# Performance work log

Hardware: AMD Instinct MI355X
Metric: run time of the kernel (lower is better)

## Reference

```python
import jax, jax.numpy as jnp
import numpy as np

DIM = 128
HEADS = 8
DH = DIM // HEADS
WIN = (4, 4, 4)
TOPK = 4
EPS = 1e-6


def _ln(x, g, b):
    mu = jnp.mean(x, -1, keepdims=True)
    var = jnp.mean((x - mu) ** 2, -1, keepdims=True)
    return (x - mu) * jax.lax.rsqrt(var + EPS) * g + b


def _win3d(x, p1, p2, p3):
    # x: [B,S,H,W,C] -> [B, p1*p2*p3, Ms, Mh, Mw, C]
    B, S, H, W, C = x.shape
    Ms, Mh, Mw = S // p1, H // p2, W // p3
    x = x.reshape(B, p1, Ms, p2, Mh, p3, Mw, C)
    x = x.transpose(0, 1, 3, 5, 2, 4, 6, 7)
    return x.reshape(B, p1 * p2 * p3, Ms, Mh, Mw, C)


def setup_inputs() -> dict:
    key = jax.random.key(0)
    ks = jax.random.split(key, 20)

    def lin(k, din, dout):
        return jax.random.normal(k, (din, dout), jnp.float32) * 0.02

    return {
        "x_in": jax.random.normal(ks[0], (2, 128, 16, 32, 32), jnp.float32),
        "x_g_in": jax.random.normal(ks[1], (2, 128, 8, 16, 16), jnp.float32),
        # Atten (global branch)
        "qkv_w": lin(ks[2], DIM, 3 * DIM), "qkv_b": jnp.zeros((3 * DIM,), jnp.float32),
        "proj_w": lin(ks[3], DIM, DIM), "proj_b": jnp.zeros((DIM,), jnp.float32),
        # shared LayerNorm (self.norm1 is reused everywhere in the original)
        "ln_g": jnp.ones((DIM,), jnp.float32), "ln_b": jnp.zeros((DIM,), jnp.float32),
        # mlp (global branch FFN)
        "mlp_w1": lin(ks[4], DIM, 4 * DIM), "mlp_b1": jnp.zeros((4 * DIM,), jnp.float32),
        "mlp_w2": lin(ks[5], 4 * DIM, DIM), "mlp_b2": jnp.zeros((DIM,), jnp.float32),
        # TopkRouting
        "rq_w": lin(ks[6], DIM, DIM), "rq_b": jnp.zeros((DIM,), jnp.float32),
        "rk_w": lin(ks[7], DIM, DIM), "rk_b": jnp.zeros((DIM,), jnp.float32),
        # fused qkv over concatenated local+gathered-global tokens
        "gqkv_w": lin(ks[8], DIM, 3 * DIM), "gqkv_b": jnp.zeros((3 * DIM,), jnp.float32),
        "wo_w": lin(ks[9], DIM, DIM), "wo_b": jnp.zeros((DIM,), jnp.float32),
        # mlp2 (local branch FFN)
        "mlp2_w1": lin(ks[10], DIM, 4 * DIM), "mlp2_b1": jnp.zeros((4 * DIM,), jnp.float32),
        "mlp2_w2": lin(ks[11], 4 * DIM, DIM), "mlp2_b2": jnp.zeros((DIM,), jnp.float32),
    }


def reference(x_in, x_g_in, qkv_w, qkv_b, proj_w, proj_b, ln_g, ln_b,
              mlp_w1, mlp_b1, mlp_w2, mlp_b2, rq_w, rq_b, rk_w, rk_b,
              gqkv_w, gqkv_b, wo_w, wo_b, mlp2_w1, mlp2_b1, mlp2_w2, mlp2_b2):
    B, C, S, H, W = x_in.shape
    Ms, Mh, Mw = WIN
    p1, p2, p3 = S // Ms, H // Mh, W // Mw  # pads are zero for these shapes
    nw, w3l = p1 * p2 * p3, Ms * Mh * Mw
    scale = DIM ** -0.5  # BiLevelRoutingAttention.scale = dim**-0.5 (not per-head)

    x = jnp.transpose(x_in, (0, 2, 3, 4, 1))  # [B,S,H,W,C]
    shortcut_l = _win3d(x, p1, p2, p3).reshape(B, nw, w3l, C)

    # ---- global branch: full self-attention + FFN ----
    _, _, gS, gH, gW = x_g_in.shape
    gN = gS * gH * gW
    xg = jnp.transpose(x_g_in, (0, 2, 3, 4, 1)).reshape(B, gN, C)
    h = _ln(xg, ln_g, ln_b)
    qkv = (h @ qkv_w + qkv_b).reshape(B, gN, 3, HEADS, DH).transpose(2, 0, 3, 1, 4)
    q, k, v = qkv[0], qkv[1], qkv[2]
    a = jax.nn.softmax(jnp.einsum('bhnd,bhmd->bhnm', q, k) * DH ** -0.5, axis=-1)
    o = jnp.einsum('bhnm,bhmd->bhnd', a, v).transpose(0, 2, 1, 3).reshape(B, gN, C)
    xg = (o @ proj_w + proj_b) + xg
    xg4 = xg.reshape(B, gS, gH, gW, C)
    h = _ln(xg4, ln_g, ln_b)
    xg4 = xg4 + (jax.nn.gelu(h @ mlp_w1 + mlp_b1, approximate=False) @ mlp_w2 + mlp_b2)

    # ---- top-k window routing ----
    swg = _win3d(xg4, p1, p2, p3)  # [B,nw,gMs,gMh,gMw,C]
    w3g = swg.shape[2] * swg.shape[3] * swg.shape[4]
    g_win = swg.mean((2, 3, 4))  # [B,nw,C]
    qh = g_win @ rq_w + rq_b
    kh = g_win @ rk_w + rk_b
    logit = jnp.einsum('bnc,bmc->bnm', qh * scale, kh)
    _tvals, tidx = jax.lax.top_k(logit, TOPK)  # r_weight is computed but unused in the original forward

    # gather top-k global windows' tokens per local window
    gflat = swg.reshape(B, nw, w3g, C)
    gath = jax.vmap(lambda kv, idx: kv[idx])(gflat, tidx)  # [B,nw,topk,w3g,C]
    sc = jnp.concatenate([shortcut_l, gath.reshape(B, nw, TOPK * w3g, C)], axis=2)
    w3 = w3l + TOPK * w3g

    # ---- local+routed attention over concatenated tokens ----
    qkvp = _ln(sc, ln_g, ln_b) @ gqkv_w + gqkv_b
    qp, kp, vp = jnp.split(qkvp, 3, axis=-1)
    qp = qp.reshape(B, nw, w3, HEADS, DH)
    kp = kp.reshape(B, nw, w3, HEADS, DH)
    vp = vp.reshape(B, nw, w3, HEADS, DH)
    aw = jax.nn.softmax(jnp.einsum('bnqhd,bnkhd->bnhqk', qp * scale, kp), axis=-1)
    out = jnp.einsum('bnhqk,bnkhd->bnqhd', aw, vp).reshape(B, nw, w3, C)

    l = out[:, :, :w3l] @ wo_w + wo_b + shortcut_l
    l = l.reshape(B, p1, p2, p3, Ms, Mh, Mw, C).transpose(0, 1, 4, 2, 5, 3, 6, 7).reshape(B, S, H, W, C)
    l = l + (jax.nn.gelu(_ln(l, ln_g, ln_b) @ mlp2_w1 + mlp2_b1, approximate=False) @ mlp2_w2 + mlp2_b2)

    l_out = jnp.transpose(l, (0, 4, 1, 2, 3))
    g_out = jnp.transpose(xg4, (0, 4, 1, 2, 3))
    return (l_out, g_out)
```

## Files before the change

kernel.cpp:

```cpp
#include <hip/hip_runtime.h>
#include <hip/hip_bf16.h>
#include <math.h>

#define BATCH 2
#define CDIM 128
#define SS 16
#define HH_ 32
#define WW_ 32
#define NSP (SS*HH_*WW_)
#define GS 8
#define GH 16
#define GW 16
#define GN (GS*GH*GW)
#define HEADS 8
#define DH 16
#define NW 256
#define W3L 64
#define W3G 8
#define TOPK 4
#define W3 (W3L + TOPK*W3G)
#define LN_EPS 1e-6f
#define ROUTE_SCALE 0.08838834764831845f
#define GATTN_SCALE 0.25f

typedef short bshort8 __attribute__((ext_vector_type(8)));
typedef float f32x4 __attribute__((ext_vector_type(4)));

__device__ __forceinline__ unsigned short f2bf(float f) {
    unsigned int u = __float_as_uint(f);
    unsigned int r = (u + 0x7fffu + ((u >> 16) & 1u)) >> 16;
    return (unsigned short)r;
}
__device__ __forceinline__ float gelu_exact(float x) {
    float z = x * 0.70710678118654752f;
    float az = fabsf(z);
    float t = 1.0f / fmaf(0.3275911f, az, 1.0f);
    float poly = t * fmaf(t, fmaf(t, fmaf(t, fmaf(t, 1.061405429f, -1.453152027f),
                     1.421413741f), -0.284496736f), 0.254829592f);
    float e = __expf(-az * az);
    float erfv = 1.0f - poly * e;
    erfv = (z < 0.f) ? -erfv : erfv;
    return 0.5f * x * (1.0f + erfv);
}
__device__ __forceinline__ float shfl_sum32(float v) {
#pragma unroll
    for (int m = 16; m > 0; m >>= 1) v += __shfl_xor(v, m);
    return v;
}
__device__ __forceinline__ float shfl_sum16(float v) {
#pragma unroll
    for (int m = 8; m > 0; m >>= 1) v += __shfl_xor(v, m);
    return v;
}
__device__ __forceinline__ float shfl_sum8(float v) {
#pragma unroll
    for (int m = 4; m > 0; m >>= 1) v += __shfl_xor(v, m);
    return v;
}

__global__ __launch_bounds__(256) void k_prep_fat(const float* __restrict__ gqkv_w,
        const float* __restrict__ m2_w1, const float* __restrict__ m2_w2,
        const float* __restrict__ proj_w, const float* __restrict__ mlp_w1,
        const float* __restrict__ mlp_w2, const float* __restrict__ wo_w,
        const float* __restrict__ qkv_w,
        unsigned short* __restrict__ wt, unsigned short* __restrict__ w1t,
        unsigned short* __restrict__ w2t, unsigned short* __restrict__ projt,
        unsigned short* __restrict__ gw1t, unsigned short* __restrict__ gw2t,
        unsigned short* __restrict__ wot, unsigned short* __restrict__ qkvt,
        const float* __restrict__ x_in, const float* __restrict__ ln_g,
        const float* __restrict__ ln_b, unsigned short* __restrict__ lnsc) {
    __shared__ float tile[16][132];
    int t = threadIdx.x;
    if (blockIdx.x < 192) {
        int id = blockIdx.x * 256 + t;
        int frag = id >> 6, lane = id & 63;
        int l15 = lane & 15, quad = lane >> 4;
        const float* srcw; unsigned short* dstw; int KS, OUT, lf; float sc = 1.f;
        if (frag < 96)        { lf = frag;       srcw = gqkv_w; dstw = wt;    KS = 4;  OUT = 384; if ((lf >> 2) < 8) sc = ROUTE_SCALE; }
        else if (frag < 224)  { lf = frag - 96;  srcw = m2_w1;  dstw = w1t;   KS = 4;  OUT = 512; }
        else if (frag < 352)  { lf = frag - 224; srcw = m2_w2;  dstw = w2t;   KS = 16; OUT = 128; }
        else if (frag < 384)  { lf = frag - 352; srcw = proj_w; dstw = projt; KS = 4;  OUT = 128; }
        else if (frag < 512)  { lf = frag - 384; srcw = mlp_w1; dstw = gw1t;  KS = 4;  OUT = 512; }
        else if (frag < 640)  { lf = frag - 512; srcw = mlp_w2; dstw = gw2t;  KS = 16; OUT = 128; }
        else if (frag < 672)  { lf = frag - 640; srcw = wo_w;   dstw = wot;   KS = 4;  OUT = 128; }
        else                  { lf = frag - 672; srcw = qkv_w;  dstw = qkvt;  KS = 4;  OUT = 384; if ((lf >> 2) < 8) sc = GATTN_SCALE; }
        int ksh = (KS == 16) ? 4 : 2;
        int tle = lf >> ksh, ks = lf & (KS - 1);
        int n = tle * 16 + l15;
        int k0 = ks * 32 + quad * 8;
        const float* s = srcw + (size_t)k0 * OUT + n;
        unsigned short o[8];
#pragma unroll
        for (int e = 0; e < 8; e++) o[e] = f2bf(s[(size_t)e * OUT] * sc);
        unsigned short* d = dstw + ((size_t)lf * 64 + lane) * 8;
        *(ushort4*)d = *(ushort4*)&o[0];
        *(ushort4*)(d + 4) = *(ushort4*)&o[4];
        return;
    }
    int blk = blockIdx.x - 192;
    int wtile = blk & 1; int hh = (blk >> 1) & 31; int s = (blk >> 6) & 15; int b = blk >> 10;
    int w0 = wtile * 16;
    {
        int c = t >> 1; int wq = (t & 1) * 8;
        const float* src = x_in + (((size_t)(b * 128 + c) * SS + s)) * 1024 + hh * 32 + w0 + wq;
        float4 v0 = *(const float4*)src;
        float4 v1 = *(const float4*)(src + 4);
        tile[wq + 0][c] = v0.x; tile[wq + 1][c] = v0.y; tile[wq + 2][c] = v0.z; tile[wq + 3][c] = v0.w;
        tile[wq + 4][c] = v1.x; tile[wq + 5][c] = v1.y; tile[wq + 6][c] = v1.z; tile[wq + 7][c] = v1.w;
    }
    __syncthreads();
    int w = t >> 4; int j = t & 15;
    float vals[8];
    float s1 = 0.f;
#pragma unroll
    for (int i = 0; i < 8; i++) { vals[i] = tile[w][j * 8 + i]; s1 += vals[i]; }
    s1 = shfl_sum16(s1);
    float mu = s1 * (1.0f / 128.0f);
    float s2 = 0.f;
#pragma unroll
    for (int i = 0; i < 8; i++) { float d = vals[i] - mu; s2 += d * d; }
    s2 = shfl_sum16(s2);
    float rs = rsqrtf(s2 * (1.0f / 128.0f) + LN_EPS);
    float4 g0 = *(const float4*)(ln_g + j * 8);
    float4 g1 = *(const float4*)(ln_g + j * 8 + 4);
    float4 b0 = *(const float4*)(ln_b + j * 8);
    float4 b1 = *(const float4*)(ln_b + j * 8 + 4);
    float gv[8] = { g0.x, g0.y, g0.z, g0.w, g1.x, g1.y, g1.z, g1.w };
    float bv[8] = { b0.x, b0.y, b0.z, b0.w, b1.x, b1.y, b1.z, b1.w };
    int ww = w0 + w;
    int n = (s >> 2) * 64 + (hh >> 2) * 8 + (ww >> 2);
    int slot = (s & 3) * 16 + (hh & 3) * 4 + (ww & 3);
    unsigned short* dst = lnsc + ((size_t)(b * NW + n) * W3 + slot) * 128 + j * 8;
    ushort4 u0, u1;
    u0.x = f2bf((vals[0] - mu) * rs * gv[0] + bv[0]);
    u0.y = f2bf((vals[1] - mu) * rs * gv[1] + bv[1]);
    u0.z = f2bf((vals[2] - mu) * rs * gv[2] + bv[2]);
    u0.w = f2bf((vals[3] - mu) * rs * gv[3] + bv[3]);
    u1.x = f2bf((vals[4] - mu) * rs * gv[4] + bv[4]);
    u1.y = f2bf((vals[5] - mu) * rs * gv[5] + bv[5]);
    u1.z = f2bf((vals[6] - mu) * rs * gv[6] + bv[6]);
    u1.w = f2bf((vals[7] - mu) * rs * gv[7] + bv[7]);
    *(ushort4*)dst = u0;
    *(ushort4*)(dst + 4) = u1;
}

__global__ __launch_bounds__(256) void k_gqkv_mfma(const float* __restrict__ xg_in,
        const unsigned short* __restrict__ qkvt, const float* __restrict__ qkv_b,
        const float* __restrict__ ln_g, const float* __restrict__ ln_b,
        float* __restrict__ xg, unsigned short* __restrict__ qgb,
        unsigned short* __restrict__ kgb, unsigned short* __restrict__ vgtb) {
    int blk = blockIdx.x; int b = blk >> 7; int n0 = (blk & 127) * 16;
    int t = threadIdx.x; int w = t >> 6; int lane = t & 63;
    int l15 = lane & 15, quad = lane >> 4;
    __shared__ __align__(16) float xs[16 * 132];
    __shared__ __align__(16) unsigned short h[16 * 136];
    f32x4 zero4 = {0.f, 0.f, 0.f, 0.f};

    {
        int c = t >> 1, j0 = (t & 1) * 8;
        const float* src = xg_in + ((size_t)(b * 128 + c)) * GN + n0 + j0;
        float4 v0 = *(const float4*)src;
        float4 v1 = *(const float4*)(src + 4);
        xs[(j0 + 0) * 132 + c] = v0.x; xs[(j0 + 1) * 132 + c] = v0.y;
        xs[(j0 + 2) * 132 + c] = v0.z; xs[(j0 + 3) * 132 + c] = v0.w;
        xs[(j0 + 4) * 132 + c] = v1.x; xs[(j0 + 5) * 132 + c] = v1.y;
        xs[(j0 + 6) * 132 + c] = v1.z; xs[(j0 + 7) * 132 + c] = v1.w;
    }
    __syncthreads();
    {
        int j = t >> 4, p = t & 15, c0 = p * 8;
        float vv[8]; float s1 = 0.f;
#pragma unroll
        for (int i = 0; i < 8; i++) { vv[i] = xs[j * 132 + c0 + i]; s1 += vv[i]; }
        s1 = shfl_sum16(s1);
        float mu = s1 * (1.0f / 128.0f);
        float s2 = 0.f;
#pragma unroll
        for (int i = 0; i < 8; i++) { float d = vv[i] - mu; s2 += d * d; }
        s2 = shfl_sum16(s2);
        float rs = rsqrtf(s2 * (1.0f / 128.0f) + LN_EPS);
        float* dst = xg + ((size_t)(b * GN) + n0 + j) * 128 + c0;
        *(float4*)dst = *(float4*)&vv[0];
        *(float4*)(dst + 4) = *(float4*)&vv[4];
        unsigned short hb[8];
#pragma unroll
        for (int i4 = 0; i4 < 2; i4++) {
            float4 g4 = *(const float4*)(ln_g + c0 + i4 * 4);
            float4 b4 = *(const float4*)(ln_b + c0 + i4 * 4);
            hb[i4 * 4 + 0] = f2bf((vv[i4 * 4 + 0] - mu) * rs * g4.x + b4.x);
            hb[i4 * 4 + 1] = f2bf((vv[i4 * 4 + 1] - mu) * rs * g4.y + b4.y);
            hb[i4 * 4 + 2] = f2bf((vv[i4 * 4 + 2] - mu) * rs * g4.z + b4.z);
            hb[i4 * 4 + 3] = f2bf((vv[i4 * 4 + 3] - mu) * rs * g4.w + b4.w);
        }
        *(ushort4*)&h[j * 136 + c0] = *(ushort4*)&hb[0];
        *(ushort4*)&h[j * 136 + c0 + 4] = *(ushort4*)&hb[4];
    }
    __syncthreads();

    bshort8 a[4];
#pragma unroll
    for (int ks = 0; ks < 4; ks++)
        a[ks] = *(const bshort8*)(h + l15 * 136 + ks * 32 + quad * 8);
    int bh_base = b * HEADS;
#pragma unroll
    for (int part = 0; part < 2; part++) {
#pragma unroll
        for (int which = 0; which < 2; which++) {
            int nt = 2 * w + which;
            f32x4 acc = zero4;
#pragma unroll
            for (int ks = 0; ks < 4; ks++) {
                bshort8 bfr = *(const bshort8*)(qkvt + (((size_t)(part * 8 + nt) * 4 + ks) * 64 + lane) * 8);
                acc = __builtin_amdgcn_mfma_f32_16x16x32_bf16(a[ks], bfr, acc, 0, 0, 0);
            }
            int ncol = part * 128 + nt * 16;
            float bias = qkv_b[ncol + l15] * (part == 0 ? GATTN_SCALE : 1.f);
            unsigned short* dst = (part == 0) ? qgb : kgb;
#pragma unroll
            for (int r = 0; r < 4; r++)
                dst[((size_t)(bh_base + nt) * GN + n0 + quad * 4 + r) * DH + l15] = f2bf(acc[r] + bias);
        }
    }
#pragma unroll
    for (int which = 0; which < 2; which++) {
        int mtv = 2 * w + which;
        f32x4 acc = zero4;
#pragma unroll
        for (int ks = 0; ks < 4; ks++) {
            bshort8 aw = *(const bshort8*)(qkvt + (((size_t)(16 + mtv) * 4 + ks) * 64 + lane) * 8);
            acc = __builtin_amdgcn_mfma_f32_16x16x32_bf16(aw, a[ks], acc, 0, 0, 0);
        }
#pragma unroll
        for (int r = 0; r < 4; r++) {
            float bias = qkv_b[256 + mtv * 16 + quad * 4 + r];
            vgtb[((size_t)(bh_base + mtv) * DH + quad * 4 + r) * GN + n0 + l15] = f2bf(acc[r] + bias);
        }
    }
}

__global__ __launch_bounds__(256) void k_gattn_mfma(const unsigned short* __restrict__ qgb,
        const unsigned short* __restrict__ kgb, const unsigned short* __restrict__ vgtb,
        float* __restrict__ og) {
    int blk = blockIdx.x;
    int bh = blk >> 7; int qt = (blk & 127) << 4;
    int b = bh >> 3, hh = bh & 7;
    int t = threadIdx.x; int w = t >> 6; int lane = t & 63;
    int col = lane & 15, quad = lane >> 4;
    __shared__ __align__(16) unsigned short Pbuf[4 * 16 * 40];
    __shared__ float po[4][64][4];
    __shared__ float pl[4][64][4];

    bshort8 aq = {0, 0, 0, 0, 0, 0, 0, 0};
    if (quad < 2)
        aq = *(const bshort8*)(qgb + ((size_t)bh * GN + qt + col) * DH + quad * 8);

    f32x4 o = {0.f, 0.f, 0.f, 0.f};
    float lsum[4] = {0.f, 0.f, 0.f, 0.f};
    const unsigned short* kb = kgb + (size_t)bh * GN * DH;
    const unsigned short* vb = vgtb + (size_t)bh * DH * GN;
    unsigned short* pb = Pbuf + w * (16 * 40);
    int row0 = quad * 4;
    int kbeg = w * 512;
    for (int kc = kbeg; kc < kbeg + 512; kc += 32) {
        bshort8 bk0 = {0, 0, 0, 0, 0, 0, 0, 0};
        bshort8 bk1 = {0, 0, 0, 0, 0, 0, 0, 0};
        if (quad < 2) {
            bk0 = *(const bshort8*)(kb + (size_t)(kc + col) * DH + quad * 8);
            bk1 = *(const bshort8*)(kb + (size_t)(kc + 16 + col) * DH + quad * 8);
        }
        f32x4 z = {0.f, 0.f, 0.f, 0.f};
        f32x4 s0 = __builtin_amdgcn_mfma_f32_16x16x32_bf16(aq, bk0, z, 0, 0, 0);
        f32x4 s1 = __builtin_amdgcn_mfma_f32_16x16x32_bf16(aq, bk1, z, 0, 0, 0);
        float p0[4], p1[4];
#pragma unroll
        for (int r = 0; r < 4; r++) {
            p0[r] = __expf(s0[r]); p1[r] = __expf(s1[r]);
            lsum[r] += p0[r] + p1[r];
        }
#pragma unroll
        for (int r = 0; r < 4; r++) {
            pb[(row0 + r) * 40 + col] = f2bf(p0[r]);
            pb[(row0 + r) * 40 + 16 + col] = f2bf(p1[r]);
        }
        bshort8 pA = *(const bshort8*)(pb + col * 40 + quad * 8);
        bshort8 bv = *(const bshort8*)(vb + (size_t)col * GN + kc + quad * 8);
        o = __builtin_amdgcn_mfma_f32_16x16x32_bf16(pA, bv, o, 0, 0, 0);
    }
#pragma unroll
    for (int r = 0; r < 4; r++) {
        float v = lsum[r];
        v += __shfl_xor(v, 1); v += __shfl_xor(v, 2);
        v += __shfl_xor(v, 4); v += __shfl_xor(v, 8);
        lsum[r] = v;
    }
#pragma unroll
    for (int r = 0; r < 4; r++) { po[w][lane][r] = o[r]; pl[w][lane][r] = lsum[r]; }
    __syncthreads();
    {
        float os = po[0][lane][w] + po[1][lane][w] + po[2][lane][w] + po[3][lane][w];
        float ls = pl[0][lane][w] + pl[1][lane][w] + pl[2][lane][w] + pl[3][lane][w];
        og[((size_t)(b * GN) + qt + quad * 4 + w) * 128 + hh * 16 + col] = os / ls;
    }
}

__global__ __launch_bounds__(256) void k_gmlp_mfma(const float* __restrict__ og,
        const float* __restrict__ xg,
        const unsigned short* __restrict__ projt, const float* __restrict__ proj_b,
        const float* __restrict__ ln_g, const float* __restrict__ ln_b,
        const unsigned short* __restrict__ gw1t, const float* __restrict__ b1,
        const unsigned short* __restrict__ gw2t, const float* __restrict__ b2,
        float* __restrict__ xg4, float* __restrict__ gout) {
    int blk = blockIdx.x; int b = blk >> 7; int n0g = (blk & 127) * 16;
    int t = threadIdx.x; int w = t >> 6; int lane = t & 63;
    int l15 = lane & 15, quad = lane >> 4;
    __shared__ __align__(16) unsigned short ao[16 * 136];
    __shared__ __align__(16) float xs[16 * 132];
    __shared__ __align__(16) unsigned short h[16 * 136];
    __shared__ __align__(16) unsigned short h1[16 * 520];
    float* of32 = (float*)h1;
    f32x4 zero4 = {0.f, 0.f, 0.f, 0.f};

    {
        int j = t >> 4, p = t & 15, c0 = p * 8;
        size_t base = ((size_t)(b * GN) + n0g + j) * 128 + c0;
        float4 v0 = *(const float4*)(og + base);
        float4 v1 = *(const float4*)(og + base + 4);
        ushort4 u0 = { f2bf(v0.x), f2bf(v0.y), f2bf(v0.z), f2bf(v0.w) };
        ushort4 u1 = { f2bf(v1.x), f2bf(v1.y), f2bf(v1.z), f2bf(v1.w) };
        *(ushort4*)&ao[j * 136 + c0] = u0;
        *(ushort4*)&ao[j * 136 + c0 + 4] = u1;
        *(float4*)&xs[j * 132 + c0] = *(const float4*)(xg + base);
        *(float4*)&xs[j * 132 + c0 + 4] = *(const float4*)(xg + base + 4);
    }
    __syncthreads();

    {
        bshort8 a[4];
#pragma unroll
        for (int ks = 0; ks < 4; ks++)
            a[ks] = *(const bshort8*)(ao + l15 * 136 + ks * 32 + quad * 8);
#pragma unroll
        for (int nt = 0; nt < 2; nt++) {
            f32x4 acc = zero4;
#pragma unroll
            for (int ks = 0; ks < 4; ks++) {
                bshort8 bfr = *(const bshort8*)(projt + (((size_t)(w * 2 + nt) * 4 + ks) * 64 + lane) * 8);
                acc = __builtin_amdgcn_mfma_f32_16x16x32_bf16(a[ks], bfr, acc, 0, 0, 0);
            }
            int n0 = w * 32 + nt * 16;
            float bias = proj_b[n0 + l15];
#pragma unroll
            for (int r = 0; r < 4; r++) {
                int m = quad * 4 + r;
                xs[m * 132 + n0 + l15] += acc[r] + bias;
            }
        }
    }
    __syncthreads();

    {
        int j = t >> 4, p = t & 15, c0 = p * 8;
        float vv[8]; float s1 = 0.f;
#pragma unroll
        for (int i = 0; i < 8; i++) { vv[i] = xs[j * 132 + c0 + i]; s1 += vv[i]; }
        s1 = shfl_sum16(s1);
        float mu = s1 * (1.0f / 128.0f);
        float s2 = 0.f;
#pragma unroll
        for (int i = 0; i < 8; i++) { float d = vv[i] - mu; s2 += d * d; }
        s2 = shfl_sum16(s2);
        float rs = rsqrtf(s2 * (1.0f / 128.0f) + LN_EPS);
        unsigned short hb[8];
#pragma unroll
        for (int i4 = 0; i4 < 2; i4++) {
            float4 g4 = *(const float4*)(ln_g + c0 + i4 * 4);
            float4 b4 = *(const float4*)(ln_b + c0 + i4 * 4);
            hb[i4 * 4 + 0] = f2bf((vv[i4 * 4 + 0] - mu) * rs * g4.x + b4.x);
            hb[i4 * 4 + 1] = f2bf((vv[i4 * 4 + 1] - mu) * rs * g4.y + b4.y);
            hb[i4 * 4 + 2] = f2bf((vv[i4 * 4 + 2] - mu) * rs * g4.z + b4.z);
            hb[i4 * 4 + 3] = f2bf((vv[i4 * 4 + 3] - mu) * rs * g4.w + b4.w);
        }
        *(ushort4*)&h[j * 136 + c0] = *(ushort4*)&hb[0];
        *(ushort4*)&h[j * 136 + c0 + 4] = *(ushort4*)&hb[4];
    }
    __syncthreads();

    {
        bshort8 a[4];
#pragma unroll
        for (int ks = 0; ks < 4; ks++)
            a[ks] = *(const bshort8*)(h + l15 * 136 + ks * 32 + quad * 8);
#pragma unroll
        for (int nt = 0; nt < 8; nt++) {
            f32x4 acc = zero4;
#pragma unroll
            for (int ks = 0; ks < 4; ks++) {
                bshort8 bfr = *(const bshort8*)(gw1t + (((size_t)(w * 8 + nt) * 4 + ks) * 64 + lane) * 8);
                acc = __builtin_amdgcn_mfma_f32_16x16x32_bf16(a[ks], bfr, acc, 0, 0, 0);
            }
            int n0 = w * 128 + nt * 16;
            float bias = b1[n0 + l15];
#pragma unroll
            for (int r = 0; r < 4; r++)
                h1[(quad * 4 + r) * 520 + n0 + l15] = f2bf(gelu_exact(acc[r] + bias));
        }
    }
    __syncthreads();

    f32x4 acc2[2]; acc2[0] = zero4; acc2[1] = zero4;
#pragma unroll 4
    for (int ks = 0; ks < 16; ks++) {
        bshort8 a = *(const bshort8*)(h1 + l15 * 520 + ks * 32 + quad * 8);
#pragma unroll
        for (int nt = 0; nt < 2; nt++) {
            bshort8 bfr = *(const bshort8*)(gw2t + (((size_t)(w * 2 + nt) * 16 + ks) * 64 + lane) * 8);
            acc2[nt] = __builtin_amdgcn_mfma_f32_16x16x32_bf16(a, bfr, acc2[nt], 0, 0, 0);
        }
    }
    __syncthreads();

    {
#pragma unroll
        for (int nt = 0; nt < 2; nt++) {
            int n0 = w * 32 + nt * 16;
            float bias = b2[n0 + l15];
#pragma unroll
            for (int r = 0; r < 4; r++) {
                int m = quad * 4 + r;
                float ov = xs[m * 132 + n0 + l15] + acc2[nt][r] + bias;
                of32[m * 132 + n0 + l15] = ov;
                xg4[((size_t)(b * GN) + n0g + m) * 128 + n0 + l15] = ov;
            }
        }
    }
    __syncthreads();

    {
        int cw = t >> 1, hf = t & 1, j0 = hf * 8;
        float* dst = gout + ((size_t)(b * 128 + cw)) * GN + n0g + j0;
#pragma unroll
        for (int i4 = 0; i4 < 2; i4++) {
            float4 ov = { of32[(j0 + i4 * 4 + 0) * 132 + cw], of32[(j0 + i4 * 4 + 1) * 132 + cw],
                          of32[(j0 + i4 * 4 + 2) * 132 + cw], of32[(j0 + i4 * 4 + 3) * 132 + cw] };
            *(float4*)(dst + i4 * 4) = ov;
        }
    }
}

__global__ void k_routing_qk(const float* __restrict__ xg4,
                             const float* __restrict__ rq_w, const float* __restrict__ rq_b,
                             const float* __restrict__ rk_w, const float* __restrict__ rk_b,
                             float* __restrict__ qh, float* __restrict__ kh) {
    int wid = blockIdx.x; int b = wid / NW, n = wid % NW;
    int c = threadIdx.x;
    int i1 = n / 64, i2 = (n / 8) % 8, i3 = n % 8;
    __shared__ float g[CDIM];
    float s = 0.f;
#pragma unroll
    for (int j = 0; j < W3G; j++) {
        int ds = j >> 2, dh = (j >> 1) & 1, dw = j & 1;
        int gi = ((i1 * 2 + ds) * GH + (i2 * 2 + dh)) * GW + (i3 * 2 + dw);
        s += xg4[((size_t)(b * GN + gi)) * CDIM + c];
    }
    g[c] = s * (1.0f / W3G);
    __syncthreads();
    float aq = rq_b[c], ak = rk_b[c];
    for (int k = 0; k < CDIM; k++) { float gv = g[k]; aq = fmaf(gv, rq_w[k * CDIM + c], aq); ak = fmaf(gv, rk_w[k * CDIM + c], ak); }
    qh[(size_t)wid * CDIM + c] = aq;
    kh[(size_t)wid * CDIM + c] = ak;
}

__global__ __launch_bounds__(256) void k_topk_gath(const float* __restrict__ qh,
        const float* __restrict__ kh, const float* __restrict__ xg4,
        const float* __restrict__ ln_g, const float* __restrict__ ln_b,
        unsigned short* __restrict__ lnsc) {
    int wid = blockIdx.x; int b = wid / NW;
    int m = threadIdx.x;
    __shared__ float q[CDIM];
    __shared__ float lv[NW];
    __shared__ int li[NW];
    __shared__ int sel4[TOPK];
    if (m < CDIM) q[m] = qh[(size_t)wid * CDIM + m] * ROUTE_SCALE;
    __syncthreads();
    float acc = 0.f;
    const float* kr = kh + ((size_t)b * NW + m) * CDIM;
    for (int k = 0; k < CDIM; k++) acc = fmaf(q[k], kr[k], acc);
#pragma unroll
    for (int sel = 0; sel < TOPK; sel++) {
        lv[m] = acc; li[m] = m; __syncthreads();
#pragma unroll
        for (int s = 128; s > 0; s >>= 1) {
            if (m < s) {
                if (lv[m + s] > lv[m] || (lv[m + s] == lv[m] && li[m + s] < li[m])) {
                    lv[m] = lv[m + s]; li[m] = li[m + s];
                }
            }
            __syncthreads();
        }
        int best = li[0]; __syncthreads();
        if (m == best) acc = -1e30f;
        if (m == 0) sel4[sel] = best;
    }
    __syncthreads();

    {
        int tt = m >> 3, p = m & 7, ch0 = p * 16;
        int kk = tt >> 3, j = tt & 7;
        int g = sel4[kk];
        int gi1 = g >> 6, gi2 = (g >> 3) & 7, gi3 = g & 7;
        int ds = j >> 2, dh = (j >> 1) & 1, dw = j & 1;
        int gi = ((gi1 * 2 + ds) * GH + (gi2 * 2 + dh)) * GW + (gi3 * 2 + dw);
        const float* src = xg4 + ((size_t)(b * GN + gi)) * CDIM + ch0;
        float4 v0 = *(const float4*)(src);
        float4 v1 = *(const float4*)(src + 4);
        float4 v2 = *(const float4*)(src + 8);
        float4 v3 = *(const float4*)(src + 12);
        float vv[16] = { v0.x, v0.y, v0.z, v0.w, v1.x, v1.y, v1.z, v1.w,
                         v2.x, v2.y, v2.z, v2.w, v3.x, v3.y, v3.z, v3.w };
        float s1 = 0.f;
#pragma unroll
        for (int i = 0; i < 16; i++) s1 += vv[i];
        s1 = shfl_sum8(s1);
        float mu = s1 * (1.0f / 128.0f);
        float s2 = 0.f;
#pragma unroll
        for (int i = 0; i < 16; i++) { float d = vv[i] - mu; s2 += d * d; }
        s2 = shfl_sum8(s2);
        float rs = rsqrtf(s2 * (1.0f / 128.0f) + LN_EPS);
        unsigned short hb[16];
#pragma unroll
        for (int i4 = 0; i4 < 4; i4++) {
            float4 g4 = *(const float4*)(ln_g + ch0 + i4 * 4);
            float4 b4 = *(const float4*)(ln_b + ch0 + i4 * 4);
            hb[i4 * 4 + 0] = f2bf((vv[i4 * 4 + 0] - mu) * rs * g4.x + b4.x);
            hb[i4 * 4 + 1] = f2bf((vv[i4 * 4 + 1] - mu) * rs * g4.y + b4.y);
            hb[i4 * 4 + 2] = f2bf((vv[i4 * 4 + 2] - mu) * rs * g4.z + b4.z);
            hb[i4 * 4 + 3] = f2bf((vv[i4 * 4 + 3] - mu) * rs * g4.w + b4.w);
        }
        unsigned short* dst = lnsc + ((size_t)wid * W3 + 64 + kk * 8 + j) * 128 + ch0;
        *(ushort4*)(dst + 0) = *(ushort4*)&hb[0];
        *(ushort4*)(dst + 4) = *(ushort4*)&hb[4];
        *(ushort4*)(dst + 8) = *(ushort4*)&hb[8];
        *(ushort4*)(dst + 12) = *(ushort4*)&hb[12];
    }
}

__global__ __launch_bounds__(512, 4) void k_local_wo_mfma(const unsigned short* __restrict__ lnsc,
        const unsigned short* __restrict__ wt, const float* __restrict__ gqkv_b,
        const unsigned short* __restrict__ wot, const float* __restrict__ wo_b,
        const float* __restrict__ x_in, float* __restrict__ lpre) {
    int wn = blockIdx.x;
    int b = wn >> 8; int n = wn & 255;
    int i1 = n >> 6, i2 = (n >> 3) & 7, i3 = n & 7;
    int s0 = i1 * 4, h0 = i2 * 4, w0 = i3 * 4;
    int t = threadIdx.x; int w = t >> 6; int lane = t & 63;
    int l15 = lane & 15, quad = lane >> 4;
    __shared__ __align__(16) unsigned short SMEM[64 * 136 + 96 * 136 + 128 * 104 + 8 * 640];
    unsigned short* Qs  = SMEM;
    unsigned short* Ks2 = SMEM + 64 * 136;
    unsigned short* Vts = SMEM + 64 * 136 + 96 * 136;
    unsigned short* Ps  = SMEM + 64 * 136 + 96 * 136 + 128 * 104;
    float* xs = (float*)Ks2;

    const unsigned short* Xb = lnsc + (size_t)wn * W3 * 128;
    f32x4 zero4 = {0.f, 0.f, 0.f, 0.f};

    int cx = t >> 2, sub = t & 3;
    float4 xr[4];
#pragma unroll
    for (int i = 0; i < 4; i++) {
        int jr = sub * 4 + i;
        int ds = jr >> 2, dh = jr & 3;
        xr[i] = *(const float4*)(x_in + ((size_t)(b * 128 + cx)) * 16384
                                 + (size_t)(s0 + ds) * 1024 + (h0 + dh) * 32 + w0);
    }

    bshort8 qw[4], kw[4], vw[4];
#pragma unroll
    for (int ks = 0; ks < 4; ks++) {
        qw[ks] = *(const bshort8*)(wt + (((size_t)(0 + w) * 4 + ks) * 64 + lane) * 8);
        kw[ks] = *(const bshort8*)(wt + (((size_t)(8 + w) * 4 + ks) * 64 + lane) * 8);
        vw[ks] = *(const bshort8*)(wt + (((size_t)(16 + w) * 4 + ks) * 64 + lane) * 8);
    }
    float qbias = gqkv_b[w * 16 + l15] * ROUTE_SCALE;
    float kbias = gqkv_b[128 + w * 16 + l15];
    float vbias[4];
#pragma unroll
    for (int r = 0; r < 4; r++) vbias[r] = gqkv_b[256 + w * 16 + quad * 4 + r];

    for (int mt = 0; mt < 6; mt++) {
        bshort8 a[4];
#pragma unroll
        for (int ks = 0; ks < 4; ks++)
            a[ks] = *(const bshort8*)(Xb + (mt * 16 + l15) * 128 + ks * 32 + quad * 8);
        f32x4 acck = zero4;
        f32x4 accv = zero4;
#pragma unroll
        for (int ks = 0; ks < 4; ks++) {
            acck = __builtin_amdgcn_mfma_f32_16x16x32_bf16(a[ks], kw[ks], acck, 0, 0, 0);
            accv = __builtin_amdgcn_mfma_f32_16x16x32_bf16(vw[ks], a[ks], accv, 0, 0, 0);
        }
#pragma unroll
        for (int r = 0; r < 4; r++) {
            Ks2[(mt * 16 + quad * 4 + r) * 136 + w * 16 + l15] = f2bf(acck[r] + kbias);
            Vts[(w * 16 + quad * 4 + r) * 104 + mt * 16 + l15] = f2bf(accv[r] + vbias[r]);
        }
        if (mt < 4) {
            f32x4 accq = zero4;
#pragma unroll
            for (int ks = 0; ks < 4; ks++)
                accq = __builtin_amdgcn_mfma_f32_16x16x32_bf16(a[ks], qw[ks], accq, 0, 0, 0);
#pragma unroll
            for (int r = 0; r < 4; r++)
                Qs[(mt * 16 + quad * 4 + r) * 136 + w * 16 + l15] = f2bf(accq[r] + qbias);
        }
    }

    unsigned short* Pw = Ps + w * 640;
    bshort8 zfrag = {0, 0, 0, 0, 0, 0, 0, 0};
    int h = w;
    for (int mt = 0; mt < 4; mt++) {
        bshort8 aq = zfrag;
        if (quad < 2)
            aq = *(const bshort8*)(Qs + (mt * 16 + l15) * 136 + h * 16 + quad * 8);
        float rsum[4] = {0.f, 0.f, 0.f, 0.f};
        f32x4 oacc = zero4;
#pragma unroll
        for (int kc = 0; kc < 96; kc += 32) {
#pragma unroll
            for (int sub2 = 0; sub2 < 2; sub2++) {
                int nt = (kc >> 4) + sub2;
                bshort8 bk = zfrag;
                if (quad < 2)
                    bk = *(const bshort8*)(Ks2 + (nt * 16 + l15) * 136 + h * 16 + quad * 8);
                f32x4 s = __builtin_amdgcn_mfma_f32_16x16x32_bf16(aq, bk, zero4, 0, 0, 0);
#pragma unroll
                for (int r = 0; r < 4; r++) {
                    float p = __expf(s[r]);
                    rsum[r] += p;
                    Pw[(quad * 4 + r) * 40 + sub2 * 16 + l15] = f2bf(p);
                }
            }
            bshort8 ap = *(const bshort8*)(Pw + l15 * 40 + quad * 8);
            bshort8 bv = *(const bshort8*)(Vts + (h * 16 + l15) * 104 + kc + quad * 8);
            oacc = __builtin_amdgcn_mfma_f32_16x16x32_bf16(ap, bv, oacc, 0, 0, 0);
        }
#pragma unroll
        for (int r = 0; r < 4; r++) {
            float v = rsum[r];
            v += __shfl_xor(v, 1); v += __shfl_xor(v, 2);
            v += __shfl_xor(v, 4); v += __shfl_xor(v, 8);
            rsum[r] = v;
        }
#pragma unroll
        for (int r = 0; r < 4; r++)
            Qs[(mt * 16 + quad * 4 + r) * 136 + h * 16 + l15] = f2bf(oacc[r] / rsum[r]);
    }

    __syncthreads();

#pragma unroll
    for (int i = 0; i < 4; i++) {
        int jr = sub * 4 + i;
        xs[(jr * 4 + 0) * 132 + cx] = xr[i].x;
        xs[(jr * 4 + 1) * 132 + cx] = xr[i].y;
        xs[(jr * 4 + 2) * 132 + cx] = xr[i].z;
        xs[(jr * 4 + 3) * 132 + cx] = xr[i].w;
    }

    float wbias = wo_b[w * 16 + l15];
    bshort8 wow[4];
#pragma unroll
    for (int ks = 0; ks < 4; ks++)
        wow[ks] = *(const bshort8*)(wot + (((size_t)w * 4 + ks) * 64 + lane) * 8);
#pragma unroll
    for (int mt = 0; mt < 4; mt++) {
        bshort8 a[4];
#pragma unroll
        for (int ks = 0; ks < 4; ks++)
            a[ks] = *(const bshort8*)(Qs + (mt * 16 + l15) * 136 + ks * 32 + quad * 8);
        f32x4 acc = zero4;
#pragma unroll
        for (int ks = 0; ks < 4; ks++)
            acc = __builtin_amdgcn_mfma_f32_16x16x32_bf16(a[ks], wow[ks], acc, 0, 0, 0);
#pragma unroll
        for (int r = 0; r < 4; r++) {
            int slot = mt * 16 + quad * 4 + r;
            int ds = slot >> 4, dh = (slot >> 2) & 3, dw = slot & 3;
            int sp = (s0 + ds) * 1024 + (h0 + dh) * 32 + (w0 + dw);
            lpre[((size_t)(b * 16384) + sp) * 128 + w * 16 + l15]
                = acc[r] + wbias + xs[slot * 132 + w * 16 + l15];
        }
    }
}

__global__ __launch_bounds__(256) void k_mlp2_mfma(const float* __restrict__ lpre,
        const float* __restrict__ ln_g, const float* __restrict__ ln_b,
        const unsigned short* __restrict__ w1t, const float* __restrict__ b1,
        const unsigned short* __restrict__ w2t, const float* __restrict__ b2,
        float* __restrict__ lout) {
    int blk = blockIdx.x;
    int T0 = blk * 32;
    int b = T0 >> 14;
    int sp = T0 & 16383;
    int t = threadIdx.x; int w = t >> 6; int lane = t & 63;
    int l15 = lane & 15, quad = lane >> 4;
    __shared__ __align__(16) unsigned short buf[32 * 520];
    float* of32 = (float*)buf;

    float res[2][2][4];
#pragma unroll
    for (int mt = 0; mt < 2; mt++)
#pragma unroll
        for (int nt = 0; nt < 2; nt++)
#pragma unroll
            for (int r = 0; r < 4; r++)
                res[mt][nt][r] = lpre[((size_t)T0 + mt * 16 + quad * 4 + r) * 128 + w * 32 + nt * 16 + l15];

    {
        int j = t >> 3, p = t & 7, c0 = p * 16;
        const float* src = lpre + ((size_t)T0 + j) * 128 + c0;
        float4 v0 = *(const float4*)(src + 0);
        float4 v1 = *(const float4*)(src + 4);
        float4 v2 = *(const float4*)(src + 8);
        float4 v3 = *(const float4*)(src + 12);
        float s1 = (v0.x + v0.y + v0.z + v0.w) + (v1.x + v1.y + v1.z + v1.w)
                 + (v2.x + v2.y + v2.z + v2.w) + (v3.x + v3.y + v3.z + v3.w);
        s1 = shfl_sum8(s1);
        float mu = s1 * (1.0f / 128.0f);
        float vv[16] = { v0.x, v0.y, v0.z, v0.w, v1.x, v1.y, v1.z, v1.w,
                         v2.x, v2.y, v2.z, v2.w, v3.x, v3.y, v3.z, v3.w };
        float s2 = 0.f;
#pragma unroll
        for (int i = 0; i < 16; i++) { float d = vv[i] - mu; s2 += d * d; }
        s2 = shfl_sum8(s2);
        float rs = rsqrtf(s2 * (1.0f / 128.0f) + LN_EPS);
        unsigned short hb[16];
#pragma unroll
        for (int i4 = 0; i4 < 4; i4++) {
            float4 g4 = *(const float4*)(ln_g + c0 + i4 * 4);
            float4 b4 = *(const float4*)(ln_b + c0 + i4 * 4);
            hb[i4 * 4 + 0] = f2bf((vv[i4 * 4 + 0] - mu) * rs * g4.x + b4.x);
            hb[i4 * 4 + 1] = f2bf((vv[i4 * 4 + 1] - mu) * rs * g4.y + b4.y);
            hb[i4 * 4 + 2] = f2bf((vv[i4 * 4 + 2] - mu) * rs * g4.z + b4.z);
            hb[i4 * 4 + 3] = f2bf((vv[i4 * 4 + 3] - mu) * rs * g4.w + b4.w);
        }
        *(ushort4*)&buf[j * 136 + c0 + 0] = *(ushort4*)&hb[0];
        *(ushort4*)&buf[j * 136 + c0 + 4] = *(ushort4*)&hb[4];
        *(ushort4*)&buf[j * 136 + c0 + 8] = *(ushort4*)&hb[8];
        *(ushort4*)&buf[j * 136 + c0 + 12] = *(ushort4*)&hb[12];
    }
    __syncthreads();

    bshort8 a1[2][4];
#pragma unroll
    for (int mt = 0; mt < 2; mt++)
#pragma unroll
        for (int ks = 0; ks < 4; ks++)
            a1[mt][ks] = *(const bshort8*)(buf + (mt * 16 + l15) * 136 + ks * 32 + quad * 8);
    __syncthreads();

    f32x4 zero4 = {0.f, 0.f, 0.f, 0.f};
    {
#pragma unroll
        for (int nt = 0; nt < 8; nt++) {
            int n0 = w * 128 + nt * 16;
            f32x4 acc0 = zero4, acc1 = zero4;
#pragma unroll
            for (int ks = 0; ks < 4; ks++) {
                bshort8 bfr = *(const bshort8*)(w1t + (((size_t)(w * 8 + nt) * 4 + ks) * 64 + lane) * 8);
                acc0 = __builtin_amdgcn_mfma_f32_16x16x32_bf16(a1[0][ks], bfr, acc0, 0, 0, 0);
                acc1 = __builtin_amdgcn_mfma_f32_16x16x32_bf16(a1[1][ks], bfr, acc1, 0, 0, 0);
            }
            float bias = b1[n0 + l15];
#pragma unroll
            for (int r = 0; r < 4; r++) {
                buf[(quad * 4 + r) * 520 + n0 + l15] = f2bf(gelu_exact(acc0[r] + bias));
                buf[(16 + quad * 4 + r) * 520 + n0 + l15] = f2bf(gelu_exact(acc1[r] + bias));
            }
        }
    }
    __syncthreads();

    f32x4 acc[2][2];
    acc[0][0] = zero4; acc[0][1] = zero4; acc[1][0] = zero4; acc[1][1] = zero4;
    {
#pragma unroll 4
        for (int ks = 0; ks < 16; ks++) {
            bshort8 a0 = *(const bshort8*)(buf + (l15) * 520 + ks * 32 + quad * 8);
            bshort8 a1b = *(const bshort8*)(buf + (16 + l15) * 520 + ks * 32 + quad * 8);
#pragma unroll
            for (int nt = 0; nt < 2; nt++) {
                bshort8 bfr = *(const bshort8*)(w2t + (((size_t)(w * 2 + nt) * 16 + ks) * 64 + lane) * 8);
                acc[0][nt] = __builtin_amdgcn_mfma_f32_16x16x32_bf16(a0, bfr, acc[0][nt], 0, 0, 0);
                acc[1][nt] = __builtin_amdgcn_mfma_f32_16x16x32_bf16(a1b, bfr, acc[1][nt], 0, 0, 0);
            }
        }
    }
    __syncthreads();

#pragma unroll
    for (int mt = 0; mt < 2; mt++) {
#pragma unroll
        for (int nt = 0; nt < 2; nt++) {
            int n0 = w * 32 + nt * 16;
            float bias = b2[n0 + l15];
#pragma unroll
            for (int r = 0; r < 4; r++) {
                int m = mt * 16 + quad * 4 + r;
                of32[m * 132 + n0 + l15] = res[mt][nt][r] + acc[mt][nt][r] + bias;
            }
        }
    }
    __syncthreads();

    {
        int c = t >> 1, half = t & 1, j0 = half * 16;
        float* dst = lout + ((size_t)(b * 128 + c)) * NSP + sp + j0;
#pragma unroll
        for (int i4 = 0; i4 < 4; i4++) {
            float4 ov = { of32[(j0 + i4 * 4 + 0) * 132 + c], of32[(j0 + i4 * 4 + 1) * 132 + c],
                          of32[(j0 + i4 * 4 + 2) * 132 + c], of32[(j0 + i4 * 4 + 3) * 132 + c] };
            *(float4*)(dst + i4 * 4) = ov;
        }
    }
}

extern "C" void kernel_launch(void* const* d_in, const int* in_sizes, int n_in,
                              void* d_out, int out_size, void* d_ws, size_t ws_size,
                              hipStream_t stream) {
    const float* x_in   = (const float*)d_in[0];
    const float* xg_in  = (const float*)d_in[1];
    const float* qkv_w  = (const float*)d_in[2];
    const float* qkv_b  = (const float*)d_in[3];
    const float* proj_w = (const float*)d_in[4];
    const float* proj_b = (const float*)d_in[5];
    const float* ln_g   = (const float*)d_in[6];
    const float* ln_b   = (const float*)d_in[7];
    const float* mlp_w1 = (const float*)d_in[8];
    const float* mlp_b1 = (const float*)d_in[9];
    const float* mlp_w2 = (const float*)d_in[10];
    const float* mlp_b2 = (const float*)d_in[11];
    const float* rq_w   = (const float*)d_in[12];
    const float* rq_b   = (const float*)d_in[13];
    const float* rk_w   = (const float*)d_in[14];
    const float* rk_b   = (const float*)d_in[15];
    const float* gqkv_w = (const float*)d_in[16];
    const float* gqkv_b = (const float*)d_in[17];
    const float* wo_w   = (const float*)d_in[18];
    const float* wo_b   = (const float*)d_in[19];
    const float* m2_w1  = (const float*)d_in[20];
    const float* m2_b1  = (const float*)d_in[21];
    const float* m2_w2  = (const float*)d_in[22];
    const float* m2_b2  = (const float*)d_in[23];

    float* out = (float*)d_out;
    float* ws  = (float*)d_ws;

    float* xg4 = ws;
    float* xg  = ws + 524288;
    unsigned short* qgb  = (unsigned short*)(ws + 1048576);
    unsigned short* kgb  = (unsigned short*)(ws + 1310720);
    unsigned short* vgtb = (unsigned short*)(ws + 1572864);
    float* og  = ws + 1835008;
    float* qh  = ws + 2359296;
    float* kh  = ws + 2424832;
    unsigned short* lnsc = (unsigned short*)(ws + 2492416);
    float* lpre = ws + 2492416 + 3145728;
    unsigned short* wt   = (unsigned short*)(ws + 14026752);
    unsigned short* w1t  = (unsigned short*)(ws + 14051328);
    unsigned short* w2t  = (unsigned short*)(ws + 14084096);
    unsigned short* projt = (unsigned short*)(ws + 14116864);
    unsigned short* gw1t  = (unsigned short*)(ws + 14125056);
    unsigned short* gw2t  = (unsigned short*)(ws + 14157824);
    unsigned short* wot   = (unsigned short*)(ws + 14190592);
    unsigned short* qkvt  = (unsigned short*)(ws + 14198784);

    const size_t L_OUT = (size_t)BATCH * CDIM * NSP;
    float* gout = out + L_OUT;

    hipLaunchKernelGGL(k_prep_fat, dim3(2240), dim3(256), 0, stream,
                       gqkv_w, m2_w1, m2_w2, proj_w, mlp_w1, mlp_w2, wo_w, qkv_w,
                       wt, w1t, w2t, projt, gw1t, gw2t, wot, qkvt,
                       x_in, ln_g, ln_b, lnsc);
    hipLaunchKernelGGL(k_gqkv_mfma, dim3(256), dim3(256), 0, stream,
                       xg_in, qkvt, qkv_b, ln_g, ln_b, xg, qgb, kgb, vgtb);
    hipLaunchKernelGGL(k_gattn_mfma, dim3(2048), dim3(256), 0, stream, qgb, kgb, vgtb, og);
    hipLaunchKernelGGL(k_gmlp_mfma, dim3(256), dim3(256), 0, stream,
                       og, xg, projt, proj_b, ln_g, ln_b, gw1t, mlp_b1, gw2t, mlp_b2,
                       xg4, gout);
    hipLaunchKernelGGL(k_routing_qk, dim3(512), dim3(128), 0, stream,
                       xg4, rq_w, rq_b, rk_w, rk_b, qh, kh);
    hipLaunchKernelGGL(k_topk_gath, dim3(512), dim3(256), 0, stream,
                       qh, kh, xg4, ln_g, ln_b, lnsc);
    hipLaunchKernelGGL(k_local_wo_mfma, dim3(512), dim3(512), 0, stream,
                       lnsc, wt, gqkv_b, wot, wo_b, x_in, lpre);
    hipLaunchKernelGGL(k_mlp2_mfma, dim3(1024), dim3(256), 0, stream,
                       lpre, ln_g, ln_b, w1t, m2_b1, w2t, m2_b2, out);
}
```

Baseline: 246.7 us.

## Fuse local window attention output projection with MLP2 in one kernel

Merges the local attention + wo projection kernel with the following LayerNorm+MLP2 kernel, so each 64-token window's pre-MLP activations stay in shared memory instead of being written to and reread from a global lpre buffer. The hidden layer is computed in two halves of 256 channels to fit within the existing shared memory, and the output is written directly in channel-major layout. This drops one kernel launch and a large global round trip, at the cost of a longer kernel with only 512 blocks (instead of 1024 for the MLP) and more syncs and register pressure.

```diff
diff --git a/kernel.cpp b/kernel.cpp
--- a/kernel.cpp
+++ b/kernel.cpp
@@ -545,10 +545,14 @@
     }
 }
 
-__global__ __launch_bounds__(512, 4) void k_local_wo_mfma(const unsigned short* __restrict__ lnsc,
+__global__ __launch_bounds__(512, 4) void k_local_full_mfma(const unsigned short* __restrict__ lnsc,
         const unsigned short* __restrict__ wt, const float* __restrict__ gqkv_b,
         const unsigned short* __restrict__ wot, const float* __restrict__ wo_b,
-        const float* __restrict__ x_in, float* __restrict__ lpre) {
+        const float* __restrict__ x_in,
+        const float* __restrict__ ln_g, const float* __restrict__ ln_b,
+        const unsigned short* __restrict__ w1t, const float* __restrict__ b1,
+        const unsigned short* __restrict__ w2t, const float* __restrict__ b2,
+        float* __restrict__ lout) {
     int wn = blockIdx.x;
     int b = wn >> 8; int n = wn & 255;
     int i1 = n >> 6, i2 = (n >> 3) & 7, i3 = n & 7;
@@ -561,6 +565,9 @@
     unsigned short* Vts = SMEM + 64 * 136 + 96 * 136;
     unsigned short* Ps  = SMEM + 64 * 136 + 96 * 136 + 128 * 104;
     float* xs = (float*)Ks2;
+    float* L  = (float*)SMEM;
+    unsigned short* H   = SMEM + 16896;
+    unsigned short* h1h = SMEM;
 
     const unsigned short* Xb = lnsc + (size_t)wn * W3 * 128;
     f32x4 zero4 = {0.f, 0.f, 0.f, 0.f};
@@ -673,6 +680,7 @@
 #pragma unroll
     for (int ks = 0; ks < 4; ks++)
         wow[ks] = *(const bshort8*)(wot + (((size_t)w * 4 + ks) * 64 + lane) * 8);
+    float res[4][4];
 #pragma unroll
     for (int mt = 0; mt < 4; mt++) {
         bshort8 a[4];
@@ -686,50 +694,31 @@
 #pragma unroll
         for (int r = 0; r < 4; r++) {
             int slot = mt * 16 + quad * 4 + r;
-            int ds = slot >> 4, dh = (slot >> 2) & 3, dw = slot & 3;
-            int sp = (s0 + ds) * 1024 + (h0 + dh) * 32 + (w0 + dw);
-            lpre[((size_t)(b * 16384) + sp) * 128 + w * 16 + l15]
-                = acc[r] + wbias + xs[slot * 132 + w * 16 + l15];
-        }
-    }
-}
-
-__global__ __launch_bounds__(256) void k_mlp2_mfma(const float* __restrict__ lpre,
-        const float* __restrict__ ln_g, const float* __restrict__ ln_b,
-        const unsigned short* __restrict__ w1t, const float* __restrict__ b1,
-        const unsigned short* __restrict__ w2t, const float* __restrict__ b2,
-        float* __restrict__ lout) {
-    int blk = blockIdx.x;
-    int T0 = blk * 32;
-    int b = T0 >> 14;
-    int sp = T0 & 16383;
-    int t = threadIdx.x; int w = t >> 6; int lane = t & 63;
-    int l15 = lane & 15, quad = lane >> 4;
-    __shared__ __align__(16) unsigned short buf[32 * 520];
-    float* of32 = (float*)buf;
-
-    float res[2][2][4];
-#pragma unroll
-    for (int mt = 0; mt < 2; mt++)
-#pragma unroll
-        for (int nt = 0; nt < 2; nt++)
-#pragma unroll
-            for (int r = 0; r < 4; r++)
-                res[mt][nt][r] = lpre[((size_t)T0 + mt * 16 + quad * 4 + r) * 128 + w * 32 + nt * 16 + l15];
-
+            res[mt][r] = acc[r] + wbias + xs[slot * 132 + w * 16 + l15];
+        }
+    }
+    __syncthreads();
+
+#pragma unroll
+    for (int mt = 0; mt < 4; mt++)
+#pragma unroll
+        for (int r = 0; r < 4; r++)
+            L[(mt * 16 + quad * 4 + r) * 132 + w * 16 + l15] = res[mt][r];
+    __syncthreads();
     {
         int j = t >> 3, p = t & 7, c0 = p * 16;
-        const float* src = lpre + ((size_t)T0 + j) * 128 + c0;
+        const float* src = L + j * 132 + c0;
         float4 v0 = *(const float4*)(src + 0);
         float4 v1 = *(const float4*)(src + 4);
         float4 v2 = *(const float4*)(src + 8);
         float4 v3 = *(const float4*)(src + 12);
-        float s1 = (v0.x + v0.y + v0.z + v0.w) + (v1.x + v1.y + v1.z + v1.w)
-                 + (v2.x + v2.y + v2.z + v2.w) + (v3.x + v3.y + v3.z + v3.w);
+        float vv[16] = { v0.x, v0.y, v0.z, v0.w, v1.x, v1.y, v1.z, v1.w,
+                         v2.x, v2.y, v2.z, v2.w, v3.x, v3.y, v3.z, v3.w };
+        float s1 = 0.f;
+#pragma unroll
+        for (int i = 0; i < 16; i++) s1 += vv[i];
         s1 = shfl_sum8(s1);
         float mu = s1 * (1.0f / 128.0f);
-        float vv[16] = { v0.x, v0.y, v0.z, v0.w, v1.x, v1.y, v1.z, v1.w,
-                         v2.x, v2.y, v2.z, v2.w, v3.x, v3.y, v3.z, v3.w };
         float s2 = 0.f;
 #pragma unroll
         for (int i = 0; i < 16; i++) { float d = vv[i] - mu; s2 += d * d; }
@@ -745,83 +734,71 @@
             hb[i4 * 4 + 2] = f2bf((vv[i4 * 4 + 2] - mu) * rs * g4.z + b4.z);
             hb[i4 * 4 + 3] = f2bf((vv[i4 * 4 + 3] - mu) * rs * g4.w + b4.w);
         }
-        *(ushort4*)&buf[j * 136 + c0 + 0] = *(ushort4*)&hb[0];
-        *(ushort4*)&buf[j * 136 + c0 + 4] = *(ushort4*)&hb[4];
-        *(ushort4*)&buf[j * 136 + c0 + 8] = *(ushort4*)&hb[8];
-        *(ushort4*)&buf[j * 136 + c0 + 12] = *(ushort4*)&hb[12];
-    }
-    __syncthreads();
-
-    bshort8 a1[2][4];
-#pragma unroll
-    for (int mt = 0; mt < 2; mt++)
-#pragma unroll
-        for (int ks = 0; ks < 4; ks++)
-            a1[mt][ks] = *(const bshort8*)(buf + (mt * 16 + l15) * 136 + ks * 32 + quad * 8);
-    __syncthreads();
-
-    f32x4 zero4 = {0.f, 0.f, 0.f, 0.f};
-    {
-#pragma unroll
-        for (int nt = 0; nt < 8; nt++) {
-            int n0 = w * 128 + nt * 16;
-            f32x4 acc0 = zero4, acc1 = zero4;
-#pragma unroll
-            for (int ks = 0; ks < 4; ks++) {
-                bshort8 bfr = *(const bshort8*)(w1t + (((size_t)(w * 8 + nt) * 4 + ks) * 64 + lane) * 8);
-                acc0 = __builtin_amdgcn_mfma_f32_16x16x32_bf16(a1[0][ks], bfr, acc0, 0, 0, 0);
-                acc1 = __builtin_amdgcn_mfma_f32_16x16x32_bf16(a1[1][ks], bfr, acc1, 0, 0, 0);
+        *(ushort4*)&H[j * 136 + c0 + 0] = *(ushort4*)&hb[0];
+        *(ushort4*)&H[j * 136 + c0 + 4] = *(ushort4*)&hb[4];
+        *(ushort4*)&H[j * 136 + c0 + 8] = *(ushort4*)&hb[8];
+        *(ushort4*)&H[j * 136 + c0 + 12] = *(ushort4*)&hb[12];
+    }
+    __syncthreads();
+
+    f32x4 acc2[4];
+#pragma unroll
+    for (int mt = 0; mt < 4; mt++) acc2[mt] = zero4;
+#pragma unroll
+    for (int half = 0; half < 2; half++) {
+#pragma unroll
+        for (int mt = 0; mt < 4; mt++) {
+            bshort8 a[4];
+#pragma unroll
+            for (int ks = 0; ks < 4; ks++)
+                a[ks] = *(const bshort8*)(H + (mt * 16 + l15) * 136 + ks * 32 + quad * 8);
+#pragma unroll
+            for (int nt = 0; nt < 2; nt++) {
+                int ctile = half * 16 + w * 2 + nt;
+                f32x4 acc = zero4;
+#pragma unroll
+                for (int ks = 0; ks < 4; ks++) {
+                    bshort8 bfr = *(const bshort8*)(w1t + (((size_t)ctile * 4 + ks) * 64 + lane) * 8);
+                    acc = __builtin_amdgcn_mfma_f32_16x16x32_bf16(a[ks], bfr, acc, 0, 0, 0);
+                }
+                float bias = b1[ctile * 16 + l15];
+#pragma unroll
+                for (int r = 0; r < 4; r++)
+                    h1h[(mt * 16 + quad * 4 + r) * 264 + w * 32 + nt * 16 + l15]
+                        = f2bf(gelu_exact(acc[r] + bias));
             }
-            float bias = b1[n0 + l15];
-#pragma unroll
-            for (int r = 0; r < 4; r++) {
-                buf[(quad * 4 + r) * 520 + n0 + l15] = f2bf(gelu_exact(acc0[r] + bias));
-                buf[(16 + quad * 4 + r) * 520 + n0 + l15] = f2bf(gelu_exact(acc1[r] + bias));
+        }
+        __syncthreads();
+#pragma unroll
+        for (int mt = 0; mt < 4; mt++) {
+#pragma unroll
+            for (int ks = 0; ks < 8; ks++) {
+                bshort8 a = *(const bshort8*)(h1h + (mt * 16 + l15) * 264 + ks * 32 + quad * 8);
+                bshort8 bfr = *(const bshort8*)(w2t + (((size_t)w * 16 + half * 8 + ks) * 64 + lane) * 8);
+                acc2[mt] = __builtin_amdgcn_mfma_f32_16x16x32_bf16(a, bfr, acc2[mt], 0, 0, 0);
             }
         }
-    }
-    __syncthreads();
-
-    f32x4 acc[2][2];
-    acc[0][0] = zero4; acc[0][1] = zero4; acc[1][0] = zero4; acc[1][1] = zero4;
-    {
-#pragma unroll 4
-        for (int ks = 0; ks < 16; ks++) {
-            bshort8 a0 = *(const bshort8*)(buf + (l15) * 520 + ks * 32 + quad * 8);
-            bshort8 a1b = *(const bshort8*)(buf + (16 + l15) * 520 + ks * 32 + quad * 8);
-#pragma unroll
-            for (int nt = 0; nt < 2; nt++) {
-                bshort8 bfr = *(const bshort8*)(w2t + (((size_t)(w * 2 + nt) * 16 + ks) * 64 + lane) * 8);
-                acc[0][nt] = __builtin_amdgcn_mfma_f32_16x16x32_bf16(a0, bfr, acc[0][nt], 0, 0, 0);
-                acc[1][nt] = __builtin_amdgcn_mfma_f32_16x16x32_bf16(a1b, bfr, acc[1][nt], 0, 0, 0);
-            }
-        }
-    }
-    __syncthreads();
-
-#pragma unroll
-    for (int mt = 0; mt < 2; mt++) {
-#pragma unroll
-        for (int nt = 0; nt < 2; nt++) {
-            int n0 = w * 32 + nt * 16;
-            float bias = b2[n0 + l15];
-#pragma unroll
-            for (int r = 0; r < 4; r++) {
-                int m = mt * 16 + quad * 4 + r;
-                of32[m * 132 + n0 + l15] = res[mt][nt][r] + acc[mt][nt][r] + bias;
-            }
-        }
-    }
-    __syncthreads();
-
-    {
-        int c = t >> 1, half = t & 1, j0 = half * 16;
-        float* dst = lout + ((size_t)(b * 128 + c)) * NSP + sp + j0;
-#pragma unroll
-        for (int i4 = 0; i4 < 4; i4++) {
-            float4 ov = { of32[(j0 + i4 * 4 + 0) * 132 + c], of32[(j0 + i4 * 4 + 1) * 132 + c],
-                          of32[(j0 + i4 * 4 + 2) * 132 + c], of32[(j0 + i4 * 4 + 3) * 132 + c] };
-            *(float4*)(dst + i4 * 4) = ov;
+        __syncthreads();
+    }
+
+    float bias2 = b2[w * 16 + l15];
+#pragma unroll
+    for (int mt = 0; mt < 4; mt++)
+#pragma unroll
+        for (int r = 0; r < 4; r++)
+            L[(mt * 16 + quad * 4 + r) * 132 + w * 16 + l15]
+                = res[mt][r] + acc2[mt][r] + bias2;
+    __syncthreads();
+    {
+        int c = t >> 2, idx = t & 3;
+        float* dstb = lout + ((size_t)(b * 128 + c)) * NSP;
+#pragma unroll
+        for (int i = 0; i < 4; i++) {
+            int jr = idx * 4 + i;
+            int ds = jr >> 2, dh = jr & 3;
+            float4 ov = { L[(jr * 4 + 0) * 132 + c], L[(jr * 4 + 1) * 132 + c],
+                          L[(jr * 4 + 2) * 132 + c], L[(jr * 4 + 3) * 132 + c] };
+            *(float4*)(dstb + (size_t)(s0 + ds) * 1024 + (h0 + dh) * 32 + w0) = ov;
         }
     }
 }
@@ -866,7 +843,6 @@
     float* qh  = ws + 2359296;
     float* kh  = ws + 2424832;
     unsigned short* lnsc = (unsigned short*)(ws + 2492416);
-    float* lpre = ws + 2492416 + 3145728;
     unsigned short* wt   = (unsigned short*)(ws + 14026752);
     unsigned short* w1t  = (unsigned short*)(ws + 14051328);
     unsigned short* w2t  = (unsigned short*)(ws + 14084096);
@@ -893,8 +869,7 @@
                        xg4, rq_w, rq_b, rk_w, rk_b, qh, kh);
     hipLaunchKernelGGL(k_topk_gath, dim3(512), dim3(256), 0, stream,
                        qh, kh, xg4, ln_g, ln_b, lnsc);
-    hipLaunchKernelGGL(k_local_wo_mfma, dim3(512), dim3(512), 0, stream,
-                       lnsc, wt, gqkv_b, wot, wo_b, x_in, lpre);
-    hipLaunchKernelGGL(k_mlp2_mfma, dim3(1024), dim3(256), 0, stream,
-                       lpre, ln_g, ln_b, w1t, m2_b1, w2t, m2_b2, out);
-}
+    hipLaunchKernelGGL(k_local_full_mfma, dim3(512), dim3(512), 0, stream,
+                       lnsc, wt, gqkv_b, wot, wo_b, x_in,
+                       ln_g, ln_b, w1t, m2_b1, w2t, m2_b2, out);
+}
```

Result: slower. 252.1 us (+2.2%).
